# Kernel tuning notes

Hardware: AMD Instinct MI355X
Metric: run time of the kernel (lower is better)

Reference implementation:

```python
import jax, jax.numpy as jnp
import numpy as np

NUM_HEADS = 16
ROPE_THETA = 10000.0


def _rope_cos_sin(seq_len, head_dim, dtype):
    # theta_i = theta^(-2i/d_k), i in [0, d_k/2)
    i = jnp.arange(head_dim // 2, dtype=jnp.float32)
    inv_freq = ROPE_THETA ** (-2.0 * i / head_dim)
    pos = jnp.arange(seq_len, dtype=jnp.float32)[:, None]
    ang = pos * inv_freq[None, :]                      # [S, d/2]
    return jnp.cos(ang).astype(dtype), jnp.sin(ang).astype(dtype)


def _apply_rope(t, cos, sin):
    # t: [B, H, S, d]; rotate consecutive pairs (complex multiply)
    B, H, S, d = t.shape
    tp = t.reshape(B, H, S, d // 2, 2)
    x0, x1 = tp[..., 0], tp[..., 1]
    r0 = x0 * cos - x1 * sin
    r1 = x0 * sin + x1 * cos
    return jnp.stack([r0, r1], axis=-1).reshape(B, H, S, d)


def setup_inputs() -> dict:
    key = jax.random.key(0)
    k1, k2, k3 = jax.random.split(key, 3)
    B, S, D = 4, 2048, 1024
    x = jax.random.normal(k1, (B, S, D), dtype=jnp.float32)
    padding_mask = jnp.ones((B, S), dtype=jnp.int32)
    # trunc-normal-ish init, std = sqrt(2/(in+out))
    std_qkv = np.sqrt(2.0 / (D + 3 * D))
    w_qkv = jax.random.normal(k2, (3 * D, D), dtype=jnp.float32) * std_qkv
    w_o = jax.random.normal(k3, (D, D), dtype=jnp.float32) * 0.02
    return {"x": x, "padding_mask": padding_mask, "w_qkv": w_qkv, "w_o": w_o}


def reference(x, padding_mask, w_qkv, w_o):
    B, S, D = x.shape
    H = NUM_HEADS
    hd = D // H
    scale = 1.0 / np.sqrt(hd)

    qkv = x @ w_qkv.T                                   # [B, S, 3D]
    q, k, v = jnp.split(qkv, 3, axis=-1)

    def to_heads(t):
        return t.reshape(B, S, H, hd).transpose(0, 2, 1, 3)  # [B, H, S, hd]

    q, k, v = to_heads(q), to_heads(k), to_heads(v)

    cos, sin = _rope_cos_sin(S, hd, x.dtype)            # [S, hd/2]
    q = _apply_rope(q, cos, sin)
    k = _apply_rope(k, cos, sin)

    scores = jnp.einsum("bhqd,bhkd->bhqk", q, k) * scale  # [B, H, S, S]

    causal = jnp.tril(jnp.ones((S, S), dtype=x.dtype))
    mask = causal[None, :, :] * padding_mask.astype(x.dtype)[:, None, :]  # [B, S, S]
    scores = jnp.where(mask[:, None, :, :] == 0, -jnp.inf, scores)

    weights = jax.nn.softmax(scores, axis=-1)
    out = jnp.einsum("bhqk,bhkd->bhqd", weights, v)     # [B, H, S, hd]
    out = out.transpose(0, 2, 1, 3).reshape(B, S, D)
    return out @ w_o.T
```

## Files before the change

### kernel.cpp

```cpp
#include <hip/hip_runtime.h>

typedef unsigned short u16;
typedef unsigned int u32;
typedef __bf16 bf16x8 __attribute__((ext_vector_type(8)));
typedef float f32x4 __attribute__((ext_vector_type(4)));

#define MFMA_BF16(a, b, c) __builtin_amdgcn_mfma_f32_16x16x32_bf16((a), (b), (c), 0, 0, 0)

#define QSCALE 0.18033688011112042f
#define M0SHIFT 24.0f

#define BARRIER __builtin_amdgcn_s_barrier()
#define LGKM0                                                \
  do {                                                       \
    asm volatile("s_waitcnt lgkmcnt(0)" ::: "memory");       \
    __builtin_amdgcn_sched_barrier(0);                       \
  } while (0)
#define WAIT_VM(N) asm volatile("s_waitcnt vmcnt(" #N ")" ::: "memory")


__device__ __forceinline__ u16 f2bf(float f) {
  u32 u = __builtin_bit_cast(u32, f);
  u += 0x7fffu + ((u >> 16) & 1u);
  return (u16)(u >> 16);
}

__device__ __forceinline__ void async_copy16(const void* g, void* l) {
  __builtin_amdgcn_global_load_lds(
      (__attribute__((address_space(1))) void*)g,
      (__attribute__((address_space(3))) void*)l, 16, 0, 0);
}


__global__ __launch_bounds__(256) void prep_kernel(
    const float* __restrict__ x_f, const float* __restrict__ wqkv_f,
    const float* __restrict__ wo_f, u16* __restrict__ xb,
    u16* __restrict__ wqkvb, u16* __restrict__ wob, float2* __restrict__ rope_t) {
  const int blk = blockIdx.x;
  if (blk < 12288) {
    const float* src;
    u16* dst;
    int base;
    float scale = 1.0f;
    if (blk < 8192)      { src = x_f;    dst = xb;    base = blk; }
    else if (blk < 11264){ src = wqkv_f; dst = wqkvb; base = blk - 8192;
                           if (base < 1024) scale = QSCALE; }
    else                 { src = wo_f;   dst = wob;   base = blk - 11264; }
    const int i = base * 1024 + threadIdx.x * 4;
    const float4 v = *(const float4*)(src + i);
    ushort4 o;
    o.x = f2bf(v.x * scale); o.y = f2bf(v.y * scale);
    o.z = f2bf(v.z * scale); o.w = f2bf(v.w * scale);
    *(ushort4*)(dst + i) = o;
  } else {
    const int idx = (blk - 12288) * 256 + threadIdx.x;
    const int s = idx >> 5, i = idx & 31;
    const float invf = __builtin_amdgcn_exp2f(-(float)i * 0.41524101186092027f);
    float rev = (float)s * invf * 0.15915494309189535f;
    rev -= floorf(rev);
    rope_t[idx] = make_float2(__builtin_amdgcn_cosf(rev), __builtin_amdgcn_sinf(rev));
  }
}


__device__ __forceinline__ void gemm256_bt(const u16* __restrict__ A,
                                           const u16* __restrict__ B,
                                           int row0, int col0, u16* lds,
                                           f32x4 acc[4][4]) {
  const int tid = threadIdx.x;
  const int wave = tid >> 6, lane = tid & 63;
  const int fr = lane & 15, quad = lane >> 4;
  const int wm = (wave >> 1) * 64;
  const int wn = (wave & 1) * 64;
  u16* bufA0 = lds;
  u16* bufB0 = lds + 16384;
  u16* bufA1 = lds + 24576;
  u16* bufB1 = lds + 40960;

  const int l8 = lane >> 3, l7 = lane & 7;
  const int csw = (l7 ^ l8) * 8;

  f32x4 zero = {0.f, 0.f, 0.f, 0.f};
#pragma unroll
  for (int mt = 0; mt < 4; ++mt)
#pragma unroll
    for (int nt = 0; nt < 4; ++nt) acc[mt][nt] = zero;

  auto stage = [&](int t) {
    u16* ba = (t & 1) ? bufA1 : bufA0;
    u16* bb = (t & 1) ? bufB1 : bufB0;
    const int k0 = t * 64;
#pragma unroll
    for (int c = 0; c < 4; ++c) {
      const int ch = c * 8 + wave;
      async_copy16(A + (size_t)(row0 + ch * 8 + l8) * 1024 + k0 + csw,
                   ba + ch * 512);
    }
#pragma unroll
    for (int c = 0; c < 2; ++c) {
      const int ch = c * 8 + wave;
      async_copy16(B + (size_t)(col0 + ch * 8 + l8) * 1024 + k0 + csw,
                   bb + ch * 512);
    }
  };

  const int f7 = fr & 7;
  const int sw0 = (quad ^ f7) * 8;
  const int sw1 = ((quad + 4) ^ f7) * 8;
  const int ar0 = (wm + fr) * 64, ar1 = (wm + 16 + fr) * 64;
  const int ar2 = (wm + 32 + fr) * 64, ar3 = (wm + 48 + fr) * 64;
  const int br0 = (wn + fr) * 64, br1 = (wn + 16 + fr) * 64;
  const int br2 = (wn + 32 + fr) * 64, br3 = (wn + 48 + fr) * 64;

  stage(0);
  stage(1);
  WAIT_VM(6);
  BARRIER;

  for (int t = 0; t < 16; ++t) {
    const u16* ba = (t & 1) ? bufA1 : bufA0;
    const u16* bb = (t & 1) ? bufB1 : bufB0;

    bf16x8 a0k0 = *(const bf16x8*)(ba + ar0 + sw0);
    bf16x8 a0k1 = *(const bf16x8*)(ba + ar0 + sw1);
    bf16x8 a1k0 = *(const bf16x8*)(ba + ar1 + sw0);
    bf16x8 a1k1 = *(const bf16x8*)(ba + ar1 + sw1);
    bf16x8 b0k0 = *(const bf16x8*)(bb + br0 + sw0);
    bf16x8 b0k1 = *(const bf16x8*)(bb + br0 + sw1);
    bf16x8 b1k0 = *(const bf16x8*)(bb + br1 + sw0);
    bf16x8 b1k1 = *(const bf16x8*)(bb + br1 + sw1);
    BARRIER;
    LGKM0;
    __builtin_amdgcn_s_setprio(1);
    acc[0][0] = MFMA_BF16(a0k0, b0k0, acc[0][0]);
    acc[0][1] = MFMA_BF16(a0k0, b1k0, acc[0][1]);
    acc[1][0] = MFMA_BF16(a1k0, b0k0, acc[1][0]);
    acc[1][1] = MFMA_BF16(a1k0, b1k0, acc[1][1]);
    acc[0][0] = MFMA_BF16(a0k1, b0k1, acc[0][0]);
    acc[0][1] = MFMA_BF16(a0k1, b1k1, acc[0][1]);
    acc[1][0] = MFMA_BF16(a1k1, b0k1, acc[1][0]);
    acc[1][1] = MFMA_BF16(a1k1, b1k1, acc[1][1]);
    __builtin_amdgcn_s_setprio(0);
    BARRIER;

    bf16x8 b2k0 = *(const bf16x8*)(bb + br2 + sw0);
    bf16x8 b2k1 = *(const bf16x8*)(bb + br2 + sw1);
    bf16x8 b3k0 = *(const bf16x8*)(bb + br3 + sw0);
    bf16x8 b3k1 = *(const bf16x8*)(bb + br3 + sw1);
    BARRIER;
    LGKM0;
    __builtin_amdgcn_s_setprio(1);
    acc[0][2] = MFMA_BF16(a0k0, b2k0, acc[0][2]);
    acc[0][3] = MFMA_BF16(a0k0, b3k0, acc[0][3]);
    acc[1][2] = MFMA_BF16(a1k0, b2k0, acc[1][2]);
    acc[1][3] = MFMA_BF16(a1k0, b3k0, acc[1][3]);
    acc[0][2] = MFMA_BF16(a0k1, b2k1, acc[0][2]);
    acc[0][3] = MFMA_BF16(a0k1, b3k1, acc[0][3]);
    acc[1][2] = MFMA_BF16(a1k1, b2k1, acc[1][2]);
    acc[1][3] = MFMA_BF16(a1k1, b3k1, acc[1][3]);
    __builtin_amdgcn_s_setprio(0);
    BARRIER;

    bf16x8 a2k0 = *(const bf16x8*)(ba + ar2 + sw0);
    bf16x8 a2k1 = *(const bf16x8*)(ba + ar2 + sw1);
    bf16x8 a3k0 = *(const bf16x8*)(ba + ar3 + sw0);
    bf16x8 a3k1 = *(const bf16x8*)(ba + ar3 + sw1);
    BARRIER;
    LGKM0;
    __builtin_amdgcn_s_setprio(1);
    acc[2][0] = MFMA_BF16(a2k0, b0k0, acc[2][0]);
    acc[2][1] = MFMA_BF16(a2k0, b1k0, acc[2][1]);
    acc[3][0] = MFMA_BF16(a3k0, b0k0, acc[3][0]);
    acc[3][1] = MFMA_BF16(a3k0, b1k0, acc[3][1]);
    acc[2][0] = MFMA_BF16(a2k1, b0k1, acc[2][0]);
    acc[2][1] = MFMA_BF16(a2k1, b1k1, acc[2][1]);
    acc[3][0] = MFMA_BF16(a3k1, b0k1, acc[3][0]);
    acc[3][1] = MFMA_BF16(a3k1, b1k1, acc[3][1]);
    acc[2][2] = MFMA_BF16(a2k0, b2k0, acc[2][2]);
    acc[2][3] = MFMA_BF16(a2k0, b3k0, acc[2][3]);
    acc[3][2] = MFMA_BF16(a3k0, b2k0, acc[3][2]);
    acc[3][3] = MFMA_BF16(a3k0, b3k0, acc[3][3]);
    acc[2][2] = MFMA_BF16(a2k1, b2k1, acc[2][2]);
    acc[2][3] = MFMA_BF16(a2k1, b3k1, acc[2][3]);
    acc[3][2] = MFMA_BF16(a3k1, b2k1, acc[3][2]);
    acc[3][3] = MFMA_BF16(a3k1, b3k1, acc[3][3]);
    __builtin_amdgcn_s_setprio(0);

    BARRIER;
    if (t + 2 < 16) {
      stage(t + 2);
      WAIT_VM(6);
    } else if (t + 2 == 16) {
      WAIT_VM(0);
    }
    BARRIER;
  }
}


__global__ __launch_bounds__(512, 2) void qkv_rope_kernel(
    const u16* __restrict__ x, const u16* __restrict__ w_qkv,
    const float2* __restrict__ rope_t,
    u16* __restrict__ q_ws, u16* __restrict__ k_ws, u16* __restrict__ vt_ws) {
  __shared__ u16 lds[49152];
  f32x4 acc[4][4];
  const int row0 = blockIdx.y * 256;
  const int col0 = blockIdx.x * 128;
  gemm256_bt(x, w_qkv, row0, col0, lds, acc);

  const int tid = threadIdx.x;
  const int wave = tid >> 6, lane = tid & 63;
  const int fr = lane & 15, quad = lane >> 4;
  const int wm = (wave >> 1) * 64, wn = (wave & 1) * 64;
  const int region = col0 >> 10;
  const int f0 = col0 & 1023;
  const int s0r = row0 & 2047;
  const int bb = row0 >> 11;
  const int h0 = f0 >> 6;


  if (region < 2) {
#pragma unroll
    for (int mt = 0; mt < 4; ++mt) {
#pragma unroll
      for (int nt = 0; nt < 4; ++nt) {
        const int n = wn + nt * 16 + fr;
        const int d = n & 63;
#pragma unroll
        for (int r = 0; r < 4; ++r) {
          const int m = wm + mt * 16 + quad * 4 + r;
          const float own = acc[mt][nt][r];
          const float part = __shfl_xor(own, 1);
          const int s = s0r + m;
          const float2 cssn = rope_t[s * 32 + (d >> 1)];
          const float val = (d & 1) ? (part * cssn.y + own * cssn.x)
                                    : (own * cssn.x - part * cssn.y);
          lds[m * 136 + n] = f2bf(val);
        }
      }
    }
    __syncthreads();
    u16* dst = (region == 0) ? q_ws : k_ws;
#pragma unroll
    for (int j = 0; j < 8; ++j) {
      const int idx2 = j * 512 + tid;
      const int m = idx2 >> 4;
      const int rem = idx2 & 15;
      const int hf = rem >> 3;
      const int c8 = (rem & 7) * 8;
      const uint4 v = *(const uint4*)(lds + m * 136 + hf * 64 + c8);
      *(uint4*)(dst + ((size_t)(bb * 16 + h0 + hf) * 2048 + s0r + m) * 64 + c8) = v;
    }
  } else {
#pragma unroll
    for (int mt = 0; mt < 4; ++mt)
#pragma unroll
      for (int nt = 0; nt < 4; ++nt) {
        const int n = wn + nt * 16 + fr;
#pragma unroll
        for (int r = 0; r < 4; ++r) {
          const int m = wm + mt * 16 + quad * 4 + r;
          lds[n * 264 + m] = f2bf(acc[mt][nt][r]);
        }
      }
    __syncthreads();
#pragma unroll
    for (int j = 0; j < 8; ++j) {
      const int idx2 = j * 512 + tid;
      const int n = idx2 >> 5;
      const int mc = (idx2 & 31) * 8;
      const int h = h0 + (n >> 6);
      const int d = n & 63;
      const uint4 v = *(const uint4*)(lds + n * 264 + mc);
      *(uint4*)(vt_ws + ((size_t)(bb * 16 + h) * 64 + d) * 2048 + s0r + mc) = v;
    }
  }
}


__global__ __launch_bounds__(256, 3) void flash_attn_kernel(
    const u16* __restrict__ Q, const u16* __restrict__ K, const u16* __restrict__ Vt,
    const int* __restrict__ pad, u16* __restrict__ O) {
  const int S = 2048;
  const int idx = blockIdx.x;
  const int bh = idx & 63;
  const int b = bh >> 4, h = bh & 15;
  const int j = (idx >> 6) & 3;
  const int sr = idx >> 8;
  const int qt_rev = (sr >> 1) * 8 + ((sr & 1) ? (7 - j) : j);
  const int q0 = (15 - qt_rev) * 128;
  const u16* Qh = Q + (size_t)bh * S * 64;
  const u16* Kh = K + (size_t)bh * S * 64;
  const u16* Vth = Vt + (size_t)bh * 64 * S;
  const int tid = threadIdx.x, wave = tid >> 6, lane = tid & 63;
  const int fr = lane & 15, quad = lane >> 4;

  __shared__ u16 lds_k[2][2 * 64 * 32];
  __shared__ u16 lds_vt[2][2 * 64 * 32];
  __shared__ u16 lds_p[4][32 * 76];
  __shared__ float lds_bias[2][64];

  const int qb = q0 + wave * 32;
  bf16x8 qfrag[2][2];
#pragma unroll
  for (int mt = 0; mt < 2; ++mt)
#pragma unroll
    for (int kk = 0; kk < 2; ++kk)
      qfrag[mt][kk] =
          *(const bf16x8*)(Qh + (size_t)(qb + mt * 16 + fr) * 64 + kk * 32 + quad * 8);

  bf16x8 ones;
#pragma unroll
  for (int jj = 0; jj < 8; ++jj) ones[jj] = (__bf16)1.0f;

  f32x4 zero = {0.f, 0.f, 0.f, 0.f};
  f32x4 o_acc[2][4], lacc[2];
#pragma unroll
  for (int mt = 0; mt < 2; ++mt) {
    lacc[mt] = zero;
#pragma unroll
    for (int nt = 0; nt < 4; ++nt) o_acc[mt][nt] = zero;
  }

  u16* pw = lds_p[wave];
  const float NEG = -__builtin_inff();

  auto stage = [&](int k0, int bufi) {
#pragma unroll
    for (int it = 0; it < 2; ++it) {
      const int slot = it * 256 + tid;
      const int row = tid >> 2;
      const int c8 = (tid & 3) * 8;
      async_copy16(Kh + (size_t)(k0 + row) * 64 + it * 32 + c8,
                   &lds_k[bufi][slot * 8]);
      async_copy16(Vth + (size_t)row * 2048 + k0 + it * 32 + c8,
                   &lds_vt[bufi][slot * 8]);
    }
    if (tid < 64) lds_bias[bufi][tid] = pad[b * S + k0 + tid] ? -M0SHIFT : NEG;
  };

  const int kend = q0 + 64;
  stage(0, 0);
  __syncthreads();
  int cur = 0;

  for (int k0 = 0; k0 <= kend; k0 += 64) {
    if (k0 < kend) stage(k0 + 64, cur ^ 1);

    if (k0 <= qb + 31) {
      const u16* lk = lds_k[cur];
      const u16* lvt = lds_vt[cur];
      const float* lb = lds_bias[cur];
      const bool needMask = (k0 + 63 > qb);
#pragma unroll
      for (int nt = 0; nt < 4; ++nt) {
        f32x4 s0 = zero, s1 = zero;
#pragma unroll
        for (int kk = 0; kk < 2; ++kk) {
          bf16x8 bfrag =
              *(const bf16x8*)(lk + (kk * 64 + nt * 16 + fr) * 32 + quad * 8);
          s0 = MFMA_BF16(qfrag[0][kk], bfrag, s0);
          s1 = MFMA_BF16(qfrag[1][kk], bfrag, s1);
        }
        const float bias = lb[nt * 16 + fr];
        const int col = k0 + nt * 16 + fr;
#pragma unroll
        for (int r = 0; r < 4; ++r) {
          float v0 = s0[r] + bias;
          float v1 = s1[r] + bias;
          if (needMask) {
            if (col > qb + quad * 4 + r) v0 = NEG;
            if (col > qb + 16 + quad * 4 + r) v1 = NEG;
          }
          const float p0 = __builtin_amdgcn_exp2f(v0);
          const float p1 = __builtin_amdgcn_exp2f(v1);
          pw[(quad * 4 + r) * 76 + nt * 16 + fr] =
              (u16)(__builtin_bit_cast(u32, p0) >> 16);
          pw[(16 + quad * 4 + r) * 76 + nt * 16 + fr] =
              (u16)(__builtin_bit_cast(u32, p1) >> 16);
        }
      }
      asm volatile("s_waitcnt lgkmcnt(0)" ::: "memory");

#pragma unroll
      for (int kk = 0; kk < 2; ++kk) {
        bf16x8 p0 = *(const bf16x8*)(pw + fr * 76 + kk * 32 + quad * 8);
        bf16x8 p1 = *(const bf16x8*)(pw + (16 + fr) * 76 + kk * 32 + quad * 8);
        lacc[0] = MFMA_BF16(p0, ones, lacc[0]);
        lacc[1] = MFMA_BF16(p1, ones, lacc[1]);
#pragma unroll
        for (int nt = 0; nt < 4; ++nt) {
          bf16x8 vf =
              *(const bf16x8*)(lvt + (kk * 64 + nt * 16 + fr) * 32 + quad * 8);
          o_acc[0][nt] = MFMA_BF16(p0, vf, o_acc[0][nt]);
          o_acc[1][nt] = MFMA_BF16(p1, vf, o_acc[1][nt]);
        }
      }
    }

    __syncthreads();
    cur ^= 1;
  }

#pragma unroll
  for (int mt = 0; mt < 2; ++mt)
#pragma unroll
    for (int r = 0; r < 4; ++r) {
      const int row = qb + mt * 16 + quad * 4 + r;
      const float l = lacc[mt][r];
      const float rl = (l > 0.f) ? (1.0f / l) : 0.f;
#pragma unroll
      for (int nt = 0; nt < 4; ++nt)
        O[(size_t)(b * S + row) * 1024 + h * 64 + nt * 16 + fr] =
            f2bf(o_acc[mt][nt][r] * rl);
    }
}


__global__ __launch_bounds__(512, 2) void oproj_kernel(
    const u16* __restrict__ A, const u16* __restrict__ w_o, float* __restrict__ out) {
  __shared__ u16 lds[49152];
  f32x4 acc[4][4];
  const int row0 = blockIdx.y * 256;
  const int col0 = blockIdx.x * 128;
  gemm256_bt(A, w_o, row0, col0, lds, acc);
  const int tid = threadIdx.x;
  const int wave = tid >> 6, lane = tid & 63;
  const int fr = lane & 15, quad = lane >> 4;
  const int wm = (wave >> 1) * 64, wn = (wave & 1) * 64;
#pragma unroll
  for (int mt = 0; mt < 4; ++mt)
#pragma unroll
    for (int nt = 0; nt < 4; ++nt) {
      const int ncol = col0 + wn + nt * 16 + fr;
#pragma unroll
      for (int r = 0; r < 4; ++r) {
        const int mrow = row0 + wm + mt * 16 + quad * 4 + r;
        out[(size_t)mrow * 1024 + ncol] = acc[mt][nt][r];
      }
    }
}


extern "C" void kernel_launch(void* const* d_in, const int* in_sizes, int n_in,
                              void* d_out, int out_size, void* d_ws, size_t ws_size,
                              hipStream_t stream) {
  const float* x_f = (const float*)d_in[0];
  const int* pad = (const int*)d_in[1];
  const float* wqkv_f = (const float*)d_in[2];
  const float* wo_f = (const float*)d_in[3];
  float* out = (float*)d_out;

  const int NX = 4 * 2048 * 1024;
  const int NWQKV = 3072 * 1024;
  const int NWO = 1024 * 1024;
  const size_t HSZ = (size_t)4 * 16 * 2048 * 64;

  u16* xb = (u16*)d_ws;
  u16* wqkvb = xb + NX;
  u16* wob = wqkvb + NWQKV;
  u16* q_ws = wob + NWO;
  u16* k_ws = q_ws + HSZ;
  u16* vt_ws = k_ws + HSZ;
  u16* attn_ws = vt_ws + HSZ;
  float2* rope_t = (float2*)(attn_ws + HSZ);

  prep_kernel<<<dim3(12544), dim3(256), 0, stream>>>(x_f, wqkv_f, wo_f, xb, wqkvb,
                                                     wob, rope_t);
  qkv_rope_kernel<<<dim3(24, 32), dim3(512), 0, stream>>>(xb, wqkvb, rope_t, q_ws,
                                                          k_ws, vt_ws);
  flash_attn_kernel<<<dim3(1024), dim3(256), 0, stream>>>(q_ws, k_ws, vt_ws, pad,
                                                          attn_ws);
  oproj_kernel<<<dim3(8, 32), dim3(512), 0, stream>>>(attn_ws, wob, out);
}
```

Measured before the change: 276.8 us.

## Rewrite flash attention inner loop with 32x32 MFMA and register-resident P

Switches the attention kernel from 16x16x32 to 32x32x16 bf16 MFMAs. S is computed transposed (K as the A operand), so the exp'd probabilities can be packed into bf16 with v_cvt_pk_bf16 and rearranged with permlane32_swap into PV operands without going through LDS. K/Vt tiles are stored with an XOR-swizzled layout to avoid bank conflicts. A per-tile ballot skips the padding-bias add when every key in the tile is valid, and setprio raises priority around the PV MFMAs. The M0SHIFT offset is removed, which drops the fixed shift from the exponent and so may change overflow headroom.

```diff
diff --git a/kernel.cpp b/kernel.cpp
--- a/kernel.cpp
+++ b/kernel.cpp
@@ -4,11 +4,13 @@
 typedef unsigned int u32;
 typedef __bf16 bf16x8 __attribute__((ext_vector_type(8)));
 typedef float f32x4 __attribute__((ext_vector_type(4)));
+typedef float f32x16 __attribute__((ext_vector_type(16)));
+typedef u32 u32x4 __attribute__((ext_vector_type(4)));
 
 #define MFMA_BF16(a, b, c) __builtin_amdgcn_mfma_f32_16x16x32_bf16((a), (b), (c), 0, 0, 0)
+#define MFMA32(a, b, c) __builtin_amdgcn_mfma_f32_32x32x16_bf16((a), (b), (c), 0, 0, 0)
 
 #define QSCALE 0.18033688011112042f
-#define M0SHIFT 24.0f
 
 #define BARRIER __builtin_amdgcn_s_barrier()
 #define LGKM0                                                \
@@ -29,6 +31,16 @@
   __builtin_amdgcn_global_load_lds(
       (__attribute__((address_space(1))) void*)g,
       (__attribute__((address_space(3))) void*)l, 16, 0, 0);
+}
+
+__device__ __forceinline__ u32 cvt_pk_bf16(float lo, float hi) {
+  u32 d;
+  asm("v_cvt_pk_bf16_f32 %0, %1, %2" : "=v"(d) : "v"(lo), "v"(hi));
+  return d;
+}
+
+__device__ __forceinline__ void swap32(u32& a, u32& b) {
+  asm("v_permlane32_swap_b32 %0, %1" : "+v"(a), "+v"(b));
 }
 
 
@@ -218,7 +230,6 @@
   const int bb = row0 >> 11;
   const int h0 = f0 >> 6;
 
-
   if (region < 2) {
 #pragma unroll
     for (int mt = 0; mt < 4; ++mt) {
@@ -293,50 +304,43 @@
   const u16* Kh = K + (size_t)bh * S * 64;
   const u16* Vth = Vt + (size_t)bh * 64 * S;
   const int tid = threadIdx.x, wave = tid >> 6, lane = tid & 63;
-  const int fr = lane & 15, quad = lane >> 4;
-
-  __shared__ u16 lds_k[2][2 * 64 * 32];
-  __shared__ u16 lds_vt[2][2 * 64 * 32];
-  __shared__ u16 lds_p[4][32 * 76];
-  __shared__ float lds_bias[2][64];
+  const int l31 = lane & 31, hi = lane >> 5, l7 = lane & 7;
+
+  __shared__ u16 lds_k[2][64 * 64];
+  __shared__ u16 lds_vt[2][64 * 64];
+  __shared__ float lds_biasf[2][64];
 
   const int qb = q0 + wave * 32;
-  bf16x8 qfrag[2][2];
-#pragma unroll
-  for (int mt = 0; mt < 2; ++mt)
-#pragma unroll
-    for (int kk = 0; kk < 2; ++kk)
-      qfrag[mt][kk] =
-          *(const bf16x8*)(Qh + (size_t)(qb + mt * 16 + fr) * 64 + kk * 32 + quad * 8);
+
+  bf16x8 qfrag[4];
+#pragma unroll
+  for (int c = 0; c < 4; ++c)
+    qfrag[c] = *(const bf16x8*)(Qh + (size_t)(qb + l31) * 64 + c * 16 + hi * 8);
 
   bf16x8 ones;
 #pragma unroll
   for (int jj = 0; jj < 8; ++jj) ones[jj] = (__bf16)1.0f;
 
-  f32x4 zero = {0.f, 0.f, 0.f, 0.f};
-  f32x4 o_acc[2][4], lacc[2];
-#pragma unroll
-  for (int mt = 0; mt < 2; ++mt) {
-    lacc[mt] = zero;
-#pragma unroll
-    for (int nt = 0; nt < 4; ++nt) o_acc[mt][nt] = zero;
-  }
-
-  u16* pw = lds_p[wave];
+  f32x16 o_acc0, o_acc1, lacc;
+#pragma unroll
+  for (int r = 0; r < 16; ++r) { o_acc0[r] = 0.f; o_acc1[r] = 0.f; lacc[r] = 0.f; }
+
   const float NEG = -__builtin_inff();
+  int pv0 = 1, pv1 = 1;
 
   auto stage = [&](int k0, int bufi) {
 #pragma unroll
     for (int it = 0; it < 2; ++it) {
       const int slot = it * 256 + tid;
-      const int row = tid >> 2;
-      const int c8 = (tid & 3) * 8;
-      async_copy16(Kh + (size_t)(k0 + row) * 64 + it * 32 + c8,
-                   &lds_k[bufi][slot * 8]);
-      async_copy16(Vth + (size_t)row * 2048 + k0 + it * 32 + c8,
-                   &lds_vt[bufi][slot * 8]);
-    }
-    if (tid < 64) lds_bias[bufi][tid] = pad[b * S + k0 + tid] ? -M0SHIFT : NEG;
+      const int row = slot >> 3;
+      const int g = slot & 7;
+      const int gs = (g ^ (row & 7)) * 8;
+      async_copy16(Kh + (size_t)(k0 + row) * 64 + gs, &lds_k[bufi][slot * 8]);
+      async_copy16(Vth + (size_t)row * 2048 + k0 + gs, &lds_vt[bufi][slot * 8]);
+    }
+    if (tid < 64) lds_biasf[bufi][tid] = pad[b * S + k0 + tid] ? 0.f : NEG;
+    const int pvn = pad[b * S + k0 + lane];
+    if (bufi) pv1 = pvn; else pv0 = pvn;
   };
 
   const int kend = q0 + 64;
@@ -350,52 +354,81 @@
     if (k0 <= qb + 31) {
       const u16* lk = lds_k[cur];
       const u16* lvt = lds_vt[cur];
-      const float* lb = lds_bias[cur];
+      const float* lb = lds_biasf[cur];
+      const int pvc = cur ? pv1 : pv0;
+      const bool fast = (__ballot(pvc != 0) == ~0ull);
       const bool needMask = (k0 + 63 > qb);
-#pragma unroll
-      for (int nt = 0; nt < 4; ++nt) {
-        f32x4 s0 = zero, s1 = zero;
-#pragma unroll
-        for (int kk = 0; kk < 2; ++kk) {
-          bf16x8 bfrag =
-              *(const bf16x8*)(lk + (kk * 64 + nt * 16 + fr) * 32 + quad * 8);
-          s0 = MFMA_BF16(qfrag[0][kk], bfrag, s0);
-          s1 = MFMA_BF16(qfrag[1][kk], bfrag, s1);
+      const int thrh = qb + l31 - k0 - 4 * hi;
+
+      f32x16 sacc0, sacc1;
+#pragma unroll
+      for (int r = 0; r < 16; ++r) { sacc0[r] = 0.f; sacc1[r] = 0.f; }
+#pragma unroll
+      for (int c = 0; c < 4; ++c) {
+        const int gsw = ((2 * c + hi) ^ l7) * 8;
+        bf16x8 kf0 = *(const bf16x8*)(lk + l31 * 64 + gsw);
+        bf16x8 kf1 = *(const bf16x8*)(lk + (l31 + 32) * 64 + gsw);
+        sacc0 = MFMA32(kf0, qfrag[c], sacc0);
+        sacc1 = MFMA32(kf1, qfrag[c], sacc1);
+      }
+
+      bf16x8 pa[2][2];
+#pragma unroll
+      for (int kt = 0; kt < 2; ++kt) {
+        float pe[16];
+        if (fast) {
+#pragma unroll
+          for (int r = 0; r < 16; ++r) {
+            float s = (kt == 0) ? sacc0[r] : sacc1[r];
+            if (needMask) {
+              const int rm = (r & 3) + 8 * (r >> 2) + 32 * kt;
+              s = (rm > thrh) ? NEG : s;
+            }
+            pe[r] = __builtin_amdgcn_exp2f(s);
+          }
+        } else {
+          f32x4 bv[4];
+#pragma unroll
+          for (int g = 0; g < 4; ++g)
+            bv[g] = *(const f32x4*)(lb + g * 8 + 4 * hi + 32 * kt);
+#pragma unroll
+          for (int r = 0; r < 16; ++r) {
+            float s = ((kt == 0) ? sacc0[r] : sacc1[r]) + bv[r >> 2][r & 3];
+            if (needMask) {
+              const int rm = (r & 3) + 8 * (r >> 2) + 32 * kt;
+              s = (rm > thrh) ? NEG : s;
+            }
+            pe[r] = __builtin_amdgcn_exp2f(s);
+          }
         }
-        const float bias = lb[nt * 16 + fr];
-        const int col = k0 + nt * 16 + fr;
-#pragma unroll
-        for (int r = 0; r < 4; ++r) {
-          float v0 = s0[r] + bias;
-          float v1 = s1[r] + bias;
-          if (needMask) {
-            if (col > qb + quad * 4 + r) v0 = NEG;
-            if (col > qb + 16 + quad * 4 + r) v1 = NEG;
-          }
-          const float p0 = __builtin_amdgcn_exp2f(v0);
-          const float p1 = __builtin_amdgcn_exp2f(v1);
-          pw[(quad * 4 + r) * 76 + nt * 16 + fr] =
-              (u16)(__builtin_bit_cast(u32, p0) >> 16);
-          pw[(16 + quad * 4 + r) * 76 + nt * 16 + fr] =
-              (u16)(__builtin_bit_cast(u32, p1) >> 16);
+        u32 a0 = cvt_pk_bf16(pe[0], pe[1]), a1 = cvt_pk_bf16(pe[2], pe[3]);
+        u32 b0 = cvt_pk_bf16(pe[4], pe[5]), b1 = cvt_pk_bf16(pe[6], pe[7]);
+        swap32(a0, b0);
+        swap32(a1, b1);
+        u32x4 w0 = {a0, a1, b0, b1};
+        pa[kt][0] = __builtin_bit_cast(bf16x8, w0);
+        u32 c0 = cvt_pk_bf16(pe[8], pe[9]), c1 = cvt_pk_bf16(pe[10], pe[11]);
+        u32 d0 = cvt_pk_bf16(pe[12], pe[13]), d1 = cvt_pk_bf16(pe[14], pe[15]);
+        swap32(c0, d0);
+        swap32(c1, d1);
+        u32x4 w1 = {c0, c1, d0, d1};
+        pa[kt][1] = __builtin_bit_cast(bf16x8, w1);
+      }
+
+      __builtin_amdgcn_s_setprio(1);
+#pragma unroll
+      for (int kt = 0; kt < 2; ++kt)
+#pragma unroll
+        for (int ks = 0; ks < 2; ++ks) {
+          const int kq = kt * 2 + ks;
+          lacc = MFMA32(pa[kt][ks], ones, lacc);
+          const int gsw = ((2 * kq + hi) ^ l7) * 8;
+          bf16x8 vf0 = *(const bf16x8*)(lvt + l31 * 64 + gsw);
+          bf16x8 vf1 = *(const bf16x8*)(lvt + (l31 + 32) * 64 + gsw);
+          o_acc0 = MFMA32(pa[kt][ks], vf0, o_acc0);
+          o_acc1 = MFMA32(pa[kt][ks], vf1, o_acc1);
         }
-      }
-      asm volatile("s_waitcnt lgkmcnt(0)" ::: "memory");
-
-#pragma unroll
-      for (int kk = 0; kk < 2; ++kk) {
-        bf16x8 p0 = *(const bf16x8*)(pw + fr * 76 + kk * 32 + quad * 8);
-        bf16x8 p1 = *(const bf16x8*)(pw + (16 + fr) * 76 + kk * 32 + quad * 8);
-        lacc[0] = MFMA_BF16(p0, ones, lacc[0]);
-        lacc[1] = MFMA_BF16(p1, ones, lacc[1]);
-#pragma unroll
-        for (int nt = 0; nt < 4; ++nt) {
-          bf16x8 vf =
-              *(const bf16x8*)(lvt + (kk * 64 + nt * 16 + fr) * 32 + quad * 8);
-          o_acc[0][nt] = MFMA_BF16(p0, vf, o_acc[0][nt]);
-          o_acc[1][nt] = MFMA_BF16(p1, vf, o_acc[1][nt]);
-        }
-      }
+      __builtin_amdgcn_s_setprio(0);
     }
 
     __syncthreads();
@@ -403,17 +436,13 @@
   }
 
 #pragma unroll
-  for (int mt = 0; mt < 2; ++mt)
-#pragma unroll
-    for (int r = 0; r < 4; ++r) {
-      const int row = qb + mt * 16 + quad * 4 + r;
-      const float l = lacc[mt][r];
-      const float rl = (l > 0.f) ? (1.0f / l) : 0.f;
-#pragma unroll
-      for (int nt = 0; nt < 4; ++nt)
-        O[(size_t)(b * S + row) * 1024 + h * 64 + nt * 16 + fr] =
-            f2bf(o_acc[mt][nt][r] * rl);
-    }
+  for (int r = 0; r < 16; ++r) {
+    const int q = qb + (r & 3) + 8 * (r >> 2) + 4 * hi;
+    const float l = lacc[r];
+    const float rl = (l > 0.f) ? (1.0f / l) : 0.f;
+    O[(size_t)(b * S + q) * 1024 + h * 64 + l31] = f2bf(o_acc0[r] * rl);
+    O[(size_t)(b * S + q) * 1024 + h * 64 + 32 + l31] = f2bf(o_acc1[r] * rl);
+  }
 }
 
 
```

Measured after the change: 251.9 us. 1.1x faster.
